# Kernel tuning notes

Measured on AMD Instinct MI355X. Metric: run time of the kernel, lower is better.

The kernel has to match this reference:

```python
import jax, jax.numpy as jnp
import numpy as np

S, B, E, H, V, L = 512, 64, 512, 768, 32000, 32
PAD_WORD, PAD_LABEL = 1, 0
PAD_BIAS = 10000.0


def _linear_init(key, fin, fout):
    # matches torch nn.Linear default U(-1/sqrt(fin), 1/sqrt(fin))
    kw, kb = jax.random.split(key)
    s = 1.0 / np.sqrt(fin)
    W = jax.random.uniform(kw, (fin, fout), minval=-s, maxval=s, dtype=jnp.float32)
    b = jax.random.uniform(kb, (fout,), minval=-s, maxval=s, dtype=jnp.float32)
    return W, b


def setup_inputs() -> dict:
    key = jax.random.key(0)
    ks = jax.random.split(key, 9)
    tokens = jax.random.randint(ks[0], (S, B), 0, V, dtype=jnp.int32)
    tags = jax.random.randint(ks[1], (S, B), 0, L, dtype=jnp.int32)
    embedding = jax.random.normal(ks[2], (V, E), dtype=jnp.float32)
    # gate order along the 4H axis: r, f, g, o (matches the 8 separate Linears, stacked)
    Wi_f, bi_f = _linear_init(ks[3], E, 4 * H)
    Wh_f, bh_f = _linear_init(ks[4], H, 4 * H)
    Wi_b, bi_b = _linear_init(ks[5], E, 4 * H)
    Wh_b, bh_b = _linear_init(ks[6], H, 4 * H)
    Wout, bout = _linear_init(ks[7], 2 * H, L)
    return {"tokens": tokens, "tags": tags, "embedding": embedding,
            "Wi_f": Wi_f, "bi_f": bi_f, "Wh_f": Wh_f, "bh_f": bh_f,
            "Wi_b": Wi_b, "bi_b": bi_b, "Wh_b": Wh_b, "bh_b": bh_b,
            "Wout": Wout, "bout": bout}


def _forward(tokens, embedding, Wi_f, bi_f, Wh_f, bh_f, Wi_b, bi_b, Wh_b, bh_b, Wout, bout):
    emb = embedding[tokens]                      # [S,B,E]
    b = tokens.shape[1]
    h = emb.shape[-1] * 0 + Wh_f.shape[0]
    # ---- forward direction: true LSTM-style recurrence ----
    xf = jnp.einsum('sbe,eg->sbg', emb, Wi_f) + bi_f   # [S,B,4H] precomputed input gates

    def step_f(carry, x):
        hid, c = carry
        g = x + hid @ Wh_f + bh_f
        r, f, gg, o = jnp.split(g, 4, axis=-1)
        c = jax.nn.sigmoid(f) * c + jax.nn.sigmoid(r) * jnp.tanh(gg)
        hid = jax.nn.sigmoid(o) * jnp.tanh(c)
        return (hid, c), hid

    z = jnp.zeros((b, h), dtype=emb.dtype)
    (hT, _), hs_f = jax.lax.scan(step_f, (z, z), xf)   # hs_f: [S,B,H]

    # ---- backward direction: source never updates `hidden`, so the hidden
    # projection uses the CONSTANT final forward hidden hT at every step.
    gb = jnp.einsum('sbe,eg->sbg', emb, Wi_b) + bi_b + hT @ Wh_b + bh_b  # [S,B,4H]
    r2, f2, g2, o2 = jnp.split(gb, 4, axis=-1)
    r2 = jax.nn.sigmoid(r2); f2 = jax.nn.sigmoid(f2)
    g2 = jnp.tanh(g2);       o2 = jax.nn.sigmoid(o2)

    def step_b(c2, gates):
        r, f, g, o = gates
        c2 = f * c2 + r * g
        return c2, o * jnp.tanh(c2)

    _, hs_b = jax.lax.scan(step_b, z, (r2, f2, g2, o2), reverse=True)  # [S,B,H], original order

    outputs = jnp.concatenate([hs_f, hs_b], axis=-1)   # [S,B,2H]
    out = outputs @ Wout + bout                        # [S,B,L]
    pad_mask = (tokens == PAD_WORD).astype(out.dtype)
    out = out.at[:, :, PAD_LABEL].add(pad_mask * PAD_BIAS)
    return out


def reference(tokens, tags, embedding, Wi_f, bi_f, Wh_f, bh_f, Wi_b, bi_b, Wh_b, bh_b, Wout, bout):
    del tags  # unused in forward, kept for signature fidelity
    return _forward(tokens, embedding, Wi_f, bi_f, Wh_f, bh_f, Wi_b, bi_b, Wh_b, bh_b, Wout, bout)
```

## Files before the change

kernel.cpp:

```cpp
#include <hip/hip_runtime.h>
#include <hip/hip_bf16.h>
#include <stdint.h>

typedef __attribute__((ext_vector_type(8))) short bf16x8;
typedef __attribute__((ext_vector_type(4))) float f32x4;
typedef __attribute__((ext_vector_type(4))) unsigned int u32x4;
typedef unsigned long long ull_t;

#define S_LEN 512
#define B_DIM 64
#define E_DIM 512
#define H_DIM 768
#define G4    3072
#define H2    1536
#define M_ROWS 32768
#define CHUNK 128
#define CM    8192
#define SLW   24
#define WPS   8
#define WPR   256
#define RWRD  4096
#define PSTR  16384
#define KRES  640
#define KREG  4
#define WROW  648
#define NTILES 1536

__device__ __forceinline__ float sigmf_(float x) { return 1.0f / (1.0f + __expf(-x)); }
__device__ __forceinline__ float tanhf2(float x) {
  x = fminf(fmaxf(x, -20.0f), 20.0f);
  float e = __expf(2.0f * x);
  return (e - 1.0f) / (e + 1.0f);
}
__device__ __forceinline__ float bfu(unsigned short u) { return __uint_as_float((unsigned)u << 16); }
__device__ __forceinline__ unsigned short packbf(float a) {
  __hip_bfloat16 t = __float2bfloat16(a);
  unsigned short b;
  __builtin_memcpy(&b, &t, 2);
  return b;
}

__global__ __launch_bounds__(256) void k_gather(const int* __restrict__ tokens,
                                                const float* __restrict__ emb,
                                                __hip_bfloat16* __restrict__ out) {
  const int t = blockIdx.x * 256 + threadIdx.x;
  const int e0 = t * 8;
  const int row = e0 >> 9;
  const int k = e0 & 511;
  const int tok = tokens[row];
  const float4* p = (const float4*)(emb + (size_t)tok * E_DIM + k);
  const float4 v0 = p[0], v1 = p[1];
  __align__(16) __hip_bfloat16 tmp[8];
  tmp[0] = __float2bfloat16(v0.x); tmp[1] = __float2bfloat16(v0.y);
  tmp[2] = __float2bfloat16(v0.z); tmp[3] = __float2bfloat16(v0.w);
  tmp[4] = __float2bfloat16(v1.x); tmp[5] = __float2bfloat16(v1.y);
  tmp[6] = __float2bfloat16(v1.z); tmp[7] = __float2bfloat16(v1.w);
  *(bf16x8*)(out + (size_t)t * 8) = *(const bf16x8*)tmp;
}

__global__ __launch_bounds__(256) void k_transpose_cast(const float* __restrict__ src,
                                                        __hip_bfloat16* __restrict__ dst,
                                                        int Rs, int Cs) {
  __shared__ float tile[32][33];
  const int tx = threadIdx.x & 31, ty = threadIdx.x >> 5;
  const int c0 = blockIdx.x * 32, r0 = blockIdx.y * 32;
  #pragma unroll
  for (int i = ty; i < 32; i += 8)
    tile[i][tx] = src[(size_t)(r0 + i) * Cs + c0 + tx];
  __syncthreads();
  #pragma unroll
  for (int i = ty; i < 32; i += 8)
    dst[(size_t)(c0 + i) * Rs + r0 + tx] = __float2bfloat16(tile[tx][i]);
}

__global__ __launch_bounds__(256) void k_bias(const float* __restrict__ bi,
                                              const float* __restrict__ bh,
                                              float* __restrict__ bias) {
  const int n = blockIdx.x * 256 + threadIdx.x;
  bias[n] = bi[n] + bh[n];
}

__device__ __forceinline__ void gemm_tile_e(char* pool, int tile,
                                            const __hip_bfloat16* __restrict__ A,
                                            const __hip_bfloat16* __restrict__ BT,
                                            const float* __restrict__ bias,
                                            __hip_bfloat16* __restrict__ C) {
  auto As = (__hip_bfloat16 (*)[40])pool;
  auto Bs = (__hip_bfloat16 (*)[40])(pool + 10240);
  const int tid = threadIdx.x;
  const int wave = tid >> 6, lane = tid & 63;
  const int q = lane >> 4, lr = lane & 15;
  const int wm = (wave >> 1) * 64, wn = (wave & 1) * 64;
  const int nb = tile % 24, mb = tile / 24;
  const int m0 = mb * 128, n0 = nb * 128;
  const int srow = tid >> 2, skseg = (tid & 3) * 8;

  f32x4 acc[4][4];
  #pragma unroll
  for (int i = 0; i < 4; ++i)
    #pragma unroll
    for (int j = 0; j < 4; ++j) { f32x4 z = {0.f, 0.f, 0.f, 0.f}; acc[i][j] = z; }

  for (int kt = 0; kt < 16; ++kt) {
    __syncthreads();
    const int kbase = kt * 32 + skseg;
    *(bf16x8*)&As[srow][skseg]      = *(const bf16x8*)(A + (size_t)(m0 + srow) * E_DIM + kbase);
    *(bf16x8*)&As[srow + 64][skseg] = *(const bf16x8*)(A + (size_t)(m0 + srow + 64) * E_DIM + kbase);
    *(bf16x8*)&Bs[srow][skseg]      = *(const bf16x8*)(BT + (size_t)(n0 + srow) * E_DIM + kbase);
    *(bf16x8*)&Bs[srow + 64][skseg] = *(const bf16x8*)(BT + (size_t)(n0 + srow + 64) * E_DIM + kbase);
    __syncthreads();
    bf16x8 af[4], bfr[4];
    #pragma unroll
    for (int mt = 0; mt < 4; ++mt) af[mt] = *(const bf16x8*)&As[wm + mt * 16 + lr][q * 8];
    #pragma unroll
    for (int nt = 0; nt < 4; ++nt) bfr[nt] = *(const bf16x8*)&Bs[wn + nt * 16 + lr][q * 8];
    #pragma unroll
    for (int mt = 0; mt < 4; ++mt)
      #pragma unroll
      for (int nt = 0; nt < 4; ++nt)
        acc[mt][nt] = __builtin_amdgcn_mfma_f32_16x16x32_bf16(af[mt], bfr[nt], acc[mt][nt], 0, 0, 0);
  }
  #pragma unroll
  for (int mt = 0; mt < 4; ++mt) {
    #pragma unroll
    for (int nt = 0; nt < 4; ++nt) {
      const int col = n0 + wn + nt * 16 + lr;
      const float bv = bias[col];
      #pragma unroll
      for (int i = 0; i < 4; ++i) {
        const int row = m0 + wm + mt * 16 + q * 4 + i;
        C[(size_t)row * G4 + col] = __float2bfloat16(acc[mt][nt][i] + bv);
      }
    }
  }
}

__device__ __forceinline__ void gemm_tile_g(char* pool, int tile,
                                            const int* __restrict__ tokens_c,
                                            const float* __restrict__ emb,
                                            const __hip_bfloat16* __restrict__ BT,
                                            const float* __restrict__ bias,
                                            __hip_bfloat16* __restrict__ C) {
  auto As = (__hip_bfloat16 (*)[40])pool;
  auto Bs = (__hip_bfloat16 (*)[40])(pool + 10240);
  const int tid = threadIdx.x;
  const int wave = tid >> 6, lane = tid & 63;
  const int q = lane >> 4, lr = lane & 15;
  const int wm = (wave >> 1) * 64, wn = (wave & 1) * 64;
  const int nb = tile % 24, mb = tile / 24;
  const int m0 = mb * 128, n0 = nb * 128;
  const int srow = tid >> 2, skseg = (tid & 3) * 8;
  const int tok0 = tokens_c[m0 + srow];
  const int tok1 = tokens_c[m0 + srow + 64];

  f32x4 acc[4][4];
  #pragma unroll
  for (int i = 0; i < 4; ++i)
    #pragma unroll
    for (int j = 0; j < 4; ++j) { f32x4 z = {0.f, 0.f, 0.f, 0.f}; acc[i][j] = z; }

  for (int kt = 0; kt < 16; ++kt) {
    __syncthreads();
    const int kbase = kt * 32 + skseg;
    {
      const float* ap = emb + (size_t)tok0 * E_DIM + kbase;
      const float4 v0 = *(const float4*)ap, v1 = *(const float4*)(ap + 4);
      __align__(16) __hip_bfloat16 t8[8];
      t8[0] = __float2bfloat16(v0.x); t8[1] = __float2bfloat16(v0.y);
      t8[2] = __float2bfloat16(v0.z); t8[3] = __float2bfloat16(v0.w);
      t8[4] = __float2bfloat16(v1.x); t8[5] = __float2bfloat16(v1.y);
      t8[6] = __float2bfloat16(v1.z); t8[7] = __float2bfloat16(v1.w);
      *(bf16x8*)&As[srow][skseg] = *(const bf16x8*)t8;
    }
    {
      const float* ap = emb + (size_t)tok1 * E_DIM + kbase;
      const float4 v0 = *(const float4*)ap, v1 = *(const float4*)(ap + 4);
      __align__(16) __hip_bfloat16 t8[8];
      t8[0] = __float2bfloat16(v0.x); t8[1] = __float2bfloat16(v0.y);
      t8[2] = __float2bfloat16(v0.z); t8[3] = __float2bfloat16(v0.w);
      t8[4] = __float2bfloat16(v1.x); t8[5] = __float2bfloat16(v1.y);
      t8[6] = __float2bfloat16(v1.z); t8[7] = __float2bfloat16(v1.w);
      *(bf16x8*)&As[srow + 64][skseg] = *(const bf16x8*)t8;
    }
    *(bf16x8*)&Bs[srow][skseg]      = *(const bf16x8*)(BT + (size_t)(n0 + srow) * E_DIM + kbase);
    *(bf16x8*)&Bs[srow + 64][skseg] = *(const bf16x8*)(BT + (size_t)(n0 + srow + 64) * E_DIM + kbase);
    __syncthreads();
    bf16x8 af[4], bfr[4];
    #pragma unroll
    for (int mt = 0; mt < 4; ++mt) af[mt] = *(const bf16x8*)&As[wm + mt * 16 + lr][q * 8];
    #pragma unroll
    for (int nt = 0; nt < 4; ++nt) bfr[nt] = *(const bf16x8*)&Bs[wn + nt * 16 + lr][q * 8];
    #pragma unroll
    for (int mt = 0; mt < 4; ++mt)
      #pragma unroll
      for (int nt = 0; nt < 4; ++nt)
        acc[mt][nt] = __builtin_amdgcn_mfma_f32_16x16x32_bf16(af[mt], bfr[nt], acc[mt][nt], 0, 0, 0);
  }
  #pragma unroll
  for (int mt = 0; mt < 4; ++mt) {
    #pragma unroll
    for (int nt = 0; nt < 4; ++nt) {
      const int col = n0 + wn + nt * 16 + lr;
      const float bv = bias[col];
      #pragma unroll
      for (int i = 0; i < 4; ++i) {
        const int row = m0 + wm + mt * 16 + q * 4 + i;
        C[(size_t)row * G4 + col] = __float2bfloat16(acc[mt][nt][i] + bv);
      }
    }
  }
}

__global__ __launch_bounds__(256) void k_gemm_e(const __hip_bfloat16* __restrict__ A,
                                                const __hip_bfloat16* __restrict__ BT,
                                                const float* __restrict__ bias,
                                                __hip_bfloat16* __restrict__ C) {
  __shared__ __align__(16) char pool[20480];
  gemm_tile_e(pool, blockIdx.x, A, BT, bias, C);
}
__global__ __launch_bounds__(256) void k_gemm_g(const int* __restrict__ tokens_c,
                                                const float* __restrict__ emb,
                                                const __hip_bfloat16* __restrict__ BT,
                                                const float* __restrict__ bias,
                                                __hip_bfloat16* __restrict__ C) {
  __shared__ __align__(16) char pool[20480];
  gemm_tile_g(pool, blockIdx.x, tokens_c, emb, BT, bias, C);
}

__device__ __forceinline__ void out_block8(char* pool, int ob,
                                           const __hip_bfloat16* __restrict__ Hs,
                                           const float* __restrict__ Wout,
                                           const float* __restrict__ bout,
                                           const int* __restrict__ tokens,
                                           float* __restrict__ out) {
  auto rowbuf = (float (*)[1536])pool;
  const int r0 = ob * 8;
  const int tid = threadIdx.x;
  for (int idx = tid; idx < 8 * 1536; idx += 256) {
    const int rr = idx / 1536, k = idx % 1536;
    rowbuf[rr][k] = __bfloat162float(Hs[(size_t)(r0 + rr) * H2 + k]);
  }
  __syncthreads();
  const int l = tid & 31, rr = tid >> 5;
  float acc = bout[l];
  #pragma unroll 8
  for (int k = 0; k < 1536; ++k) acc += rowbuf[rr][k] * Wout[k * 32 + l];
  const int row = r0 + rr;
  if (l == 0 && tokens[row] == 1) acc += 10000.0f;
  out[(size_t)row * 32 + l] = acc;
  __syncthreads();
}

__global__ __launch_bounds__(256) void k_out(const __hip_bfloat16* __restrict__ Hs,
                                             const float* __restrict__ Wout,
                                             const float* __restrict__ bout,
                                             const int* __restrict__ tokens,
                                             float* __restrict__ out) {
  __shared__ __align__(16) char pool[49152];
  out_block8(pool, blockIdx.x, Hs, Wout, bout, tokens, out);
}

__global__ __launch_bounds__(256, 1) void k_fwd_fused(const __hip_bfloat16* __restrict__ X,
                                                      const __hip_bfloat16* __restrict__ WhTf,
                                                      ull_t* __restrict__ hbuf,
                                                      __hip_bfloat16* __restrict__ Hs,
                                                      float* __restrict__ cstate,
                                                      float* __restrict__ hT,
                                                      int chunk,
                                                      const __hip_bfloat16* __restrict__ EmbA,
                                                      const int* __restrict__ tokens_nx,
                                                      const float* __restrict__ emb,
                                                      const __hip_bfloat16* __restrict__ WiT_nx,
                                                      const float* __restrict__ Bias_nx,
                                                      __hip_bfloat16* __restrict__ Xw) {
  __shared__ __align__(16) char pool[155904];
  const int bx = blockIdx.x;

  if (bx >= 128) {
    const int nw = gridDim.x - 128;
    if (EmbA) {
      for (int t = bx - 128; t < NTILES; t += nw)
        gemm_tile_e(pool, t, EmbA, WiT_nx, Bias_nx, Xw);
    } else {
      for (int t = bx - 128; t < NTILES; t += nw)
        gemm_tile_g(pool, t, tokens_nx, emb, WiT_nx, Bias_nx, Xw);
    }
    return;
  }

  unsigned short* wlds = (unsigned short*)pool;
  auto h_stage = (unsigned short (*)[776])(pool + 124416);
  auto g_lds   = (float (*)[16][26])(pool + 149248);

  const int group = bx >> 5;
  const int slice = bx & 31;
  const int r0 = group * 16;
  const int j0 = slice * SLW;
  const int tid = threadIdx.x;
  const int w = tid >> 6;
  const int lane = tid & 63;
  const int q = lane >> 4, lr = lane & 15;
  const int base = chunk * CHUNK;

  const int prow = tid >> 4;
  const int pw   = tid & 15;

  const int row  = tid >> 3;
  const int wloc = tid & 7;
  const int col0 = 3 * wloc;

  for (int c = tid; c < 96 * (KRES / 8); c += 256) {
    const int r = c / (KRES / 8), k8 = c % (KRES / 8);
    const int gate = r / SLW, n = r % SLW;
    const float4 v = *(const float4*)(WhTf + (size_t)(gate * H_DIM + j0 + n) * H_DIM + k8 * 8);
    *(float4*)(wlds + (size_t)r * WROW + k8 * 8) = v;
  }

  const int wn0 = lr;
  const int wn1 = 16 + (lr & 7);
  bf16x8 wr0[KREG], wr1[KREG];
  #pragma unroll
  for (int kk = 0; kk < KREG; ++kk) {
    const int ko = KRES + kk * 32 + q * 8;
    wr0[kk] = *(const bf16x8*)(WhTf + (size_t)(w * H_DIM + j0 + wn0) * H_DIM + ko);
    wr1[kk] = *(const bf16x8*)(WhTf + (size_t)(w * H_DIM + j0 + wn1) * H_DIM + ko);
  }

  float cr[3] = {0.f, 0.f, 0.f};
  if (tid < 128) {
    const float* cs = cstate + (size_t)(r0 + row) * H_DIM + j0 + col0;
    cr[0] = cs[0]; cr[1] = cs[1]; cr[2] = cs[2];
  }

  const unsigned skipbit = ((pw >> 2) == (slice & 3)) ? (1u << (slice >> 2)) : 0u;

  __syncthreads();

  for (int s = 0; s < CHUNK; ++s) {
    const int gs = base + s;

    unsigned short xs[4][3];
    if (tid < 128) {
      const unsigned short* xp = (const unsigned short*)(X + ((size_t)s * B_DIM + r0 + row) * G4 + j0 + col0);
      #pragma unroll
      for (int g = 0; g < 4; ++g)
        #pragma unroll
        for (int j = 0; j < 3; ++j) xs[g][j] = xp[g * H_DIM + j];
    }

    const ull_t* hc = hbuf + ((size_t)(gs & 1)) * PSTR + (size_t)group * RWRD
                    + (size_t)prow * WPR + 2 * pw;
    u32x4 d0 = {0,0,0,0}, d1 = {0,0,0,0}, d2 = {0,0,0,0}, d3 = {0,0,0,0};
    u32x4 d4 = {0,0,0,0}, d5 = {0,0,0,0}, d6 = {0,0,0,0}, d7 = {0,0,0,0};
    const unsigned pollmask = (s == 0) ? 0xFFu : (0xFFu ^ skipbit);
    {
      const unsigned e16 = (unsigned)(unsigned short)gs;
      unsigned need = pollmask;
      long guard = 0;
      for (;;) {
#define POLL_LD(i, dv) \
        if (need & (1u << (i))) \
          asm volatile("global_load_dwordx4 %0, %1, off sc0 sc1" \
                       : "=v"(dv) : "v"(hc + 32 * (i)) : "memory");
        POLL_LD(0, d0) POLL_LD(1, d1) POLL_LD(2, d2) POLL_LD(3, d3)
        POLL_LD(4, d4) POLL_LD(5, d5) POLL_LD(6, d6) POLL_LD(7, d7)
#undef POLL_LD
        asm volatile("s_waitcnt vmcnt(0)"
                     : "+v"(d0), "+v"(d1), "+v"(d2), "+v"(d3),
                       "+v"(d4), "+v"(d5), "+v"(d6), "+v"(d7)
                     :: "memory");
        unsigned nn = 0;
#define POLL_CK(i, dv) \
        if ((need & (1u << (i))) && \
            ((((dv).x & 0xFFFFu) != e16) || (((dv).z & 0xFFFFu) != e16))) nn |= 1u << (i);
        POLL_CK(0, d0) POLL_CK(1, d1) POLL_CK(2, d2) POLL_CK(3, d3)
        POLL_CK(4, d4) POLL_CK(5, d5) POLL_CK(6, d6) POLL_CK(7, d7)
#undef POLL_CK
        need = nn;
        if (!need) break;
        if (++guard > (1L << 20)) break;
        __builtin_amdgcn_s_sleep(1);
      }
    }
    {
#define STAGE_PAIR(i, dv) \
      if (pollmask & (1u << (i))) { \
        unsigned* hp = (unsigned*)&h_stage[prow][6 * pw + 96 * (i)]; \
        hp[0] = ((dv).x >> 16) | ((dv).y << 16); \
        hp[1] = ((dv).y >> 16) | ((dv).z & 0xFFFF0000u); \
        hp[2] = (dv).w; \
      }
      STAGE_PAIR(0, d0) STAGE_PAIR(1, d1) STAGE_PAIR(2, d2) STAGE_PAIR(3, d3)
      STAGE_PAIR(4, d4) STAGE_PAIR(5, d5) STAGE_PAIR(6, d6) STAGE_PAIR(7, d7)
#undef STAGE_PAIR
    }
    __syncthreads();

    f32x4 acc0 = {0.f, 0.f, 0.f, 0.f};
    f32x4 acc1 = {0.f, 0.f, 0.f, 0.f};
    {
      const unsigned short* wb = wlds + (size_t)w * SLW * WROW;
      #pragma unroll
      for (int kt = 0; kt < KRES / 32; ++kt) {
        const int ko = kt * 32 + q * 8;
        const bf16x8 a  = *(const bf16x8*)&h_stage[lr][ko];
        const bf16x8 b0 = *(const bf16x8*)(wb + (size_t)wn0 * WROW + ko);
        const bf16x8 b1 = *(const bf16x8*)(wb + (size_t)wn1 * WROW + ko);
        acc0 = __builtin_amdgcn_mfma_f32_16x16x32_bf16(a, b0, acc0, 0, 0, 0);
        acc1 = __builtin_amdgcn_mfma_f32_16x16x32_bf16(a, b1, acc1, 0, 0, 0);
      }
      #pragma unroll
      for (int kk = 0; kk < KREG; ++kk) {
        const bf16x8 a = *(const bf16x8*)&h_stage[lr][KRES + kk * 32 + q * 8];
        acc0 = __builtin_amdgcn_mfma_f32_16x16x32_bf16(a, wr0[kk], acc0, 0, 0, 0);
        acc1 = __builtin_amdgcn_mfma_f32_16x16x32_bf16(a, wr1[kk], acc1, 0, 0, 0);
      }
    }
    #pragma unroll
    for (int i = 0; i < 4; ++i) g_lds[w][q * 4 + i][lr] = acc0[i];
    if (lr < 8) {
      #pragma unroll
      for (int i = 0; i < 4; ++i) g_lds[w][q * 4 + i][16 + lr] = acc1[i];
    }
    __syncthreads();

    if (tid < 128) {
      float h[3];
      #pragma unroll
      for (int j = 0; j < 3; ++j) {
        const float rv = g_lds[0][row][col0 + j] + bfu(xs[0][j]);
        const float fv = g_lds[1][row][col0 + j] + bfu(xs[1][j]);
        const float gv = g_lds[2][row][col0 + j] + bfu(xs[2][j]);
        const float ov = g_lds[3][row][col0 + j] + bfu(xs[3][j]);
        const float c = sigmf_(fv) * cr[j] + sigmf_(rv) * tanhf2(gv);
        cr[j] = c;
        h[j] = sigmf_(ov) * tanhf2(c);
      }
      const unsigned short b0 = packbf(h[0]), b1 = packbf(h[1]), b2 = packbf(h[2]);
      const ull_t wv = (ull_t)(unsigned short)(gs + 1)
                     | ((ull_t)b0 << 16) | ((ull_t)b1 << 32) | ((ull_t)b2 << 48);
      __hip_atomic_store(hbuf + ((size_t)((gs + 1) & 1)) * PSTR + (size_t)group * RWRD
                         + (size_t)row * WPR + slice * WPS + wloc,
                         wv, __ATOMIC_RELAXED, __HIP_MEMORY_SCOPE_AGENT);
      h_stage[row][j0 + col0]     = b0;
      h_stage[row][j0 + col0 + 1] = b1;
      h_stage[row][j0 + col0 + 2] = b2;
      unsigned short* hsp = (unsigned short*)(Hs + ((size_t)gs * B_DIM + r0 + row) * H2 + j0 + col0);
      hsp[0] = b0; hsp[1] = b1; hsp[2] = b2;
      if (chunk == 3 && s == CHUNK - 1) {
        float* hp = hT + (size_t)(r0 + row) * H_DIM + j0 + col0;
        hp[0] = h[0]; hp[1] = h[1]; hp[2] = h[2];
      }
    }
  }

  if (tid < 128) {
    float* cs = cstate + (size_t)(r0 + row) * H_DIM + j0 + col0;
    cs[0] = cr[0]; cs[1] = cr[1]; cs[2] = cr[2];
  }
}

__global__ __launch_bounds__(256) void k_hTW(const float* __restrict__ hT,
                                             const float* __restrict__ Whb,
                                             float* __restrict__ hTW) {
  const int b = blockIdx.y;
  const int n = blockIdx.x * 256 + threadIdx.x;
  __shared__ float hs[768];
  for (int i = threadIdx.x; i < 768; i += 256) hs[i] = hT[b * 768 + i];
  __syncthreads();
  float acc = 0.f;
  #pragma unroll 4
  for (int k = 0; k < 768; ++k) acc += hs[k] * Whb[(size_t)k * G4 + n];
  hTW[(size_t)b * G4 + n] = acc;
}

__global__ __launch_bounds__(256) void k_bwd_fused(const __hip_bfloat16* __restrict__ X,
                                                   const float* __restrict__ hTW,
                                                   __hip_bfloat16* __restrict__ Hs,
                                                   float* __restrict__ c2state,
                                                   int chunk,
                                                   const __hip_bfloat16* __restrict__ EmbB,
                                                   const int* __restrict__ tokens_nx,
                                                   const float* __restrict__ emb,
                                                   const __hip_bfloat16* __restrict__ WiTb,
                                                   const float* __restrict__ BiasB,
                                                   __hip_bfloat16* __restrict__ Xw,
                                                   int do_gemm, int out_chunk,
                                                   const float* __restrict__ Wout,
                                                   const float* __restrict__ bout,
                                                   const int* __restrict__ tokens_all,
                                                   float* __restrict__ out) {
  __shared__ __align__(16) char pool[49152];
  const int bx = blockIdx.x;

  if (bx >= 640) {
    if (out_chunk >= 0)
      for (int ob = bx - 640; ob < 1024; ob += 128)
        out_block8(pool, out_chunk * 1024 + ob, Hs, Wout, bout, tokens_all, out);
    return;
  }
  if (bx >= 192) {
    if (do_gemm) {
      if (EmbB) {
        for (int t = bx - 192; t < NTILES; t += 448)
          gemm_tile_e(pool, t, EmbB, WiTb, BiasB, Xw);
      } else {
        for (int t = bx - 192; t < NTILES; t += 448)
          gemm_tile_g(pool, t, tokens_nx, emb, WiTb, BiasB, Xw);
      }
    }
    return;
  }

  const int t = bx * 256 + threadIdx.x;
  const int b = t / H_DIM;
  const int j = t % H_DIM;
  const int base = chunk * CHUNK;
  const float hw0 = hTW[(size_t)b * G4 + j];
  const float hw1 = hTW[(size_t)b * G4 + 768 + j];
  const float hw2 = hTW[(size_t)b * G4 + 1536 + j];
  const float hw3 = hTW[(size_t)b * G4 + 2304 + j];
  float c2 = c2state[t];
  for (int s = CHUNK - 1; s >= 0; --s) {
    const size_t xb = ((size_t)s * B_DIM + b) * G4 + j;
    const float r = sigmf_(__bfloat162float(X[xb]) + hw0);
    const float f = sigmf_(__bfloat162float(X[xb + 768]) + hw1);
    const float g = tanhf2(__bfloat162float(X[xb + 1536]) + hw2);
    const float o = sigmf_(__bfloat162float(X[xb + 2304]) + hw3);
    c2 = f * c2 + r * g;
    Hs[((size_t)(base + s) * B_DIM + b) * H2 + H_DIM + j] = __float2bfloat16(o * tanhf2(c2));
  }
  c2state[t] = c2;
}

extern "C" void kernel_launch(void* const* d_in, const int* in_sizes, int n_in,
                              void* d_out, int out_size, void* d_ws, size_t ws_size,
                              hipStream_t stream) {
  const int*   tokens = (const int*)d_in[0];
  const float* emb    = (const float*)d_in[2];
  const float* Wi_f   = (const float*)d_in[3];
  const float* bi_f   = (const float*)d_in[4];
  const float* Wh_f   = (const float*)d_in[5];
  const float* bh_f   = (const float*)d_in[6];
  const float* Wi_b   = (const float*)d_in[7];
  const float* bi_b   = (const float*)d_in[8];
  const float* Wh_b   = (const float*)d_in[9];
  const float* bh_b   = (const float*)d_in[10];
  const float* Wout   = (const float*)d_in[11];
  const float* bout   = (const float*)d_in[12];
  float* out = (float*)d_out;
  char* ws = (char*)d_ws;

  size_t off = 0;
  auto alloc = [&](size_t bytes) { size_t o = off; off += (bytes + 255) & ~(size_t)255; return o; };
  const size_t oHs    = alloc((size_t)M_ROWS * H2 * 2);
  const size_t oX0    = alloc((size_t)CM * G4 * 2);
  const size_t oWhTf  = alloc((size_t)G4 * H_DIM * 2);
  const size_t oWiTf  = alloc((size_t)G4 * E_DIM * 2);
  const size_t oWiTb  = alloc((size_t)G4 * E_DIM * 2);
  const size_t oBiasF = alloc((size_t)G4 * 4);
  const size_t oBiasB = alloc((size_t)G4 * 4);
  const size_t oHbuf  = alloc((size_t)2 * PSTR * 8);
  const size_t oCst   = alloc((size_t)B_DIM * H_DIM * 4);
  const size_t oHT    = alloc((size_t)B_DIM * H_DIM * 4);
  const size_t oHTW   = alloc((size_t)B_DIM * G4 * 4);
  const size_t oC2    = alloc((size_t)B_DIM * H_DIM * 4);
  const size_t oX1    = alloc((size_t)CM * G4 * 2);
  const bool overlap = (off <= ws_size);
  const size_t oEmb   = alloc((size_t)M_ROWS * E_DIM * 2);
  const bool tierA = (off <= ws_size);
  (void)in_sizes; (void)n_in; (void)out_size;

  __hip_bfloat16* Hs   = (__hip_bfloat16*)(ws + oHs);
  __hip_bfloat16* X0   = (__hip_bfloat16*)(ws + oX0);
  __hip_bfloat16* X1   = overlap ? (__hip_bfloat16*)(ws + oX1) : X0;
  __hip_bfloat16* Emb  = tierA ? (__hip_bfloat16*)(ws + oEmb) : (__hip_bfloat16*)nullptr;
  __hip_bfloat16* WhTf = (__hip_bfloat16*)(ws + oWhTf);
  __hip_bfloat16* WiTf = (__hip_bfloat16*)(ws + oWiTf);
  __hip_bfloat16* WiTb = (__hip_bfloat16*)(ws + oWiTb);
  float*          BiasF= (float*)(ws + oBiasF);
  float*          BiasB= (float*)(ws + oBiasB);
  ull_t*          Hbuf = (ull_t*)(ws + oHbuf);
  float*          Cst  = (float*)(ws + oCst);
  float*          HT   = (float*)(ws + oHT);
  float*          HTW  = (float*)(ws + oHTW);
  float*          C2   = (float*)(ws + oC2);

  hipMemsetAsync(ws + oHbuf, 0, (size_t)2 * PSTR * 8, stream);
  hipMemsetAsync(ws + oCst, 0, (size_t)B_DIM * H_DIM * 4, stream);
  hipMemsetAsync(ws + oC2, 0, (size_t)B_DIM * H_DIM * 4, stream);

  if (tierA)
    k_gather<<<8192, 256, 0, stream>>>(tokens, emb, Emb);
  k_transpose_cast<<<dim3(96, 24), 256, 0, stream>>>(Wh_f, WhTf, 768, 3072);
  k_transpose_cast<<<dim3(96, 16), 256, 0, stream>>>(Wi_f, WiTf, 512, 3072);
  k_transpose_cast<<<dim3(96, 16), 256, 0, stream>>>(Wi_b, WiTb, 512, 3072);
  k_bias<<<12, 256, 0, stream>>>(bi_f, bh_f, BiasF);
  k_bias<<<12, 256, 0, stream>>>(bi_b, bh_b, BiasB);

  if (overlap) {
    if (tierA) k_gemm_e<<<NTILES, 256, 0, stream>>>(Emb, WiTf, BiasF, X0);
    else       k_gemm_g<<<NTILES, 256, 0, stream>>>(tokens, emb, WiTf, BiasF, X0);
    auto EA = [&](int c) { return tierA ? Emb + (size_t)c * CM * E_DIM : (__hip_bfloat16*)nullptr; };
    k_fwd_fused<<<240, 256, 0, stream>>>(X0, WhTf, Hbuf, Hs, Cst, HT, 0,
                                         EA(1), tokens + 1 * CM, emb, WiTf, BiasF, X1);
    k_fwd_fused<<<240, 256, 0, stream>>>(X1, WhTf, Hbuf, Hs, Cst, HT, 1,
                                         EA(2), tokens + 2 * CM, emb, WiTf, BiasF, X0);
    k_fwd_fused<<<240, 256, 0, stream>>>(X0, WhTf, Hbuf, Hs, Cst, HT, 2,
                                         EA(3), tokens + 3 * CM, emb, WiTf, BiasF, X1);
    k_fwd_fused<<<240, 256, 0, stream>>>(X1, WhTf, Hbuf, Hs, Cst, HT, 3,
                                         EA(3), tokens + 3 * CM, emb, WiTb, BiasB, X0);
    k_hTW<<<dim3(12, 64), 256, 0, stream>>>(HT, Wh_b, HTW);
    k_bwd_fused<<<768, 256, 0, stream>>>(X0, HTW, Hs, C2, 3,
                                         EA(2), tokens + 2 * CM, emb, WiTb, BiasB, X1, 1, -1,
                                         Wout, bout, tokens, out);
    k_bwd_fused<<<768, 256, 0, stream>>>(X1, HTW, Hs, C2, 2,
                                         EA(1), tokens + 1 * CM, emb, WiTb, BiasB, X0, 1, 3,
                                         Wout, bout, tokens, out);
    k_bwd_fused<<<768, 256, 0, stream>>>(X0, HTW, Hs, C2, 1,
                                         EA(0), tokens + 0 * CM, emb, WiTb, BiasB, X1, 1, 2,
                                         Wout, bout, tokens, out);
    k_bwd_fused<<<768, 256, 0, stream>>>(X1, HTW, Hs, C2, 0,
                                         EA(0), tokens, emb, WiTb, BiasB, X0, 0, 1,
                                         Wout, bout, tokens, out);
    k_out<<<1024, 256, 0, stream>>>(Hs, Wout, bout, tokens, out);
  } else {
    for (int c = 0; c < 4; ++c) {
      k_gemm_g<<<NTILES, 256, 0, stream>>>(tokens + (size_t)c * CM, emb, WiTf, BiasF, X0);
      k_fwd_fused<<<128, 256, 0, stream>>>(X0, WhTf, Hbuf, Hs, Cst, HT, c,
                                           nullptr, tokens, emb, WiTf, BiasF, X0);
    }
    k_hTW<<<dim3(12, 64), 256, 0, stream>>>(HT, Wh_b, HTW);
    for (int c = 3; c >= 0; --c) {
      k_gemm_g<<<NTILES, 256, 0, stream>>>(tokens + (size_t)c * CM, emb, WiTb, BiasB, X0);
      k_bwd_fused<<<192, 256, 0, stream>>>(X0, HTW, Hs, C2, c,
                                           nullptr, tokens, emb, WiTb, BiasB, X0, 0, -1,
                                           Wout, bout, tokens, out);
    }
    k_out<<<4096, 256, 0, stream>>>(Hs, Wout, bout, tokens, out);
  }
}
```

Baseline: 3.292 ms.

## Fuse backward input-gate GEMM into backward scan, dropping X gate buffer

Replaces the backward pass, which first materialised the input-gate projection X and then scanned it, with a kernel that keeps a 96x512 slice of Wi_b resident in LDS. At each step pair it loads embeddings and computes the gate pre-activations with MFMA before applying the cell update in place. This removes the global write and reread of the large bf16 gate tensor and the separate GEMM tiles in the backward pass. In exchange it uses about 143 KB of LDS per block, runs one block per CU, and serialises each step on block-wide barriers. The separate backward GEMM is also no longer prefetched by the last forward launch.

```diff
diff --git a/kernel.cpp b/kernel.cpp
--- a/kernel.cpp
+++ b/kernel.cpp
@@ -25,6 +25,7 @@
 #define KREG  4
 #define WROW  648
 #define NTILES 1536
+#define EROW  520
 
 __device__ __forceinline__ float sigmf_(float x) { return 1.0f / (1.0f + __expf(-x)); }
 __device__ __forceinline__ float tanhf2(float x) {
@@ -474,45 +475,139 @@
   hTW[(size_t)b * G4 + n] = acc;
 }
 
-__global__ __launch_bounds__(256) void k_bwd_fused(const __hip_bfloat16* __restrict__ X,
-                                                   const float* __restrict__ hTW,
-                                                   __hip_bfloat16* __restrict__ Hs,
-                                                   float* __restrict__ c2state,
-                                                   int chunk,
-                                                   const __hip_bfloat16* __restrict__ EmbB,
-                                                   const int* __restrict__ tokens_nx,
-                                                   const float* __restrict__ emb,
-                                                   const __hip_bfloat16* __restrict__ WiTb,
-                                                   const float* __restrict__ BiasB,
-                                                   __hip_bfloat16* __restrict__ Xw,
-                                                   int do_gemm, int out_chunk,
-                                                   const float* __restrict__ Wout,
-                                                   const float* __restrict__ bout,
-                                                   const int* __restrict__ tokens_all,
-                                                   float* __restrict__ out) {
-  __shared__ __align__(16) char pool[49152];
+__global__ __launch_bounds__(256, 1) void k_bwd_fused2(const __hip_bfloat16* __restrict__ Emb,
+                                                       const __hip_bfloat16* __restrict__ WiTb,
+                                                       const float* __restrict__ BiasB,
+                                                       const float* __restrict__ hTW,
+                                                       __hip_bfloat16* __restrict__ Hs,
+                                                       float* __restrict__ c2state,
+                                                       int chunk, int out_chunk,
+                                                       const float* __restrict__ Wout,
+                                                       const float* __restrict__ bout,
+                                                       const int* __restrict__ tokens,
+                                                       float* __restrict__ out) {
+  __shared__ __align__(16) char pool[146432];
   const int bx = blockIdx.x;
 
-  if (bx >= 640) {
+  if (bx >= 128) {
     if (out_chunk >= 0)
-      for (int ob = bx - 640; ob < 1024; ob += 128)
-        out_block8(pool, out_chunk * 1024 + ob, Hs, Wout, bout, tokens_all, out);
+      for (int ob = bx - 128; ob < 1024; ob += 128)
+        out_block8(pool, out_chunk * 1024 + ob, Hs, Wout, bout, tokens, out);
     return;
   }
-  if (bx >= 192) {
-    if (do_gemm) {
-      if (EmbB) {
-        for (int t = bx - 192; t < NTILES; t += 448)
-          gemm_tile_e(pool, t, EmbB, WiTb, BiasB, Xw);
-      } else {
-        for (int t = bx - 192; t < NTILES; t += 448)
-          gemm_tile_g(pool, t, tokens_nx, emb, WiTb, BiasB, Xw);
-      }
-    }
-    return;
-  }
-
-  const int t = bx * 256 + threadIdx.x;
+
+  unsigned short* wlds = (unsigned short*)pool;
+  auto emb_s = (unsigned short (*)[EROW])(pool + 99840);
+  auto g_lds = (float (*)[2][16][26])(pool + 133120);
+
+  const int group = bx >> 5;
+  const int slice = bx & 31;
+  const int r0 = group * 16;
+  const int j0 = slice * SLW;
+  const int tid = threadIdx.x;
+  const int w = tid >> 6;
+  const int lane = tid & 63;
+  const int q = lane >> 4, lr = lane & 15;
+  const int base = chunk * CHUNK;
+
+  for (int c = tid; c < 96 * 64; c += 256) {
+    const int r = c >> 6, k8 = c & 63;
+    const int gate = r / SLW, n = r % SLW;
+    *(float4*)(wlds + (size_t)r * EROW + k8 * 8) =
+        *(const float4*)(WiTb + (size_t)(gate * H_DIM + j0 + n) * E_DIM + k8 * 8);
+  }
+
+  const int row = tid >> 3, wloc = tid & 7, col0 = 3 * wloc;
+  float hw0[3], hw1[3], hw2[3], hw3[3], c2r[3] = {0.f, 0.f, 0.f};
+  if (tid < 128) {
+    const int b = r0 + row;
+    #pragma unroll
+    for (int j = 0; j < 3; ++j) {
+      const int n = j0 + col0 + j;
+      hw0[j] = BiasB[n]        + hTW[(size_t)b * G4 + n];
+      hw1[j] = BiasB[768 + n]  + hTW[(size_t)b * G4 + 768 + n];
+      hw2[j] = BiasB[1536 + n] + hTW[(size_t)b * G4 + 1536 + n];
+      hw3[j] = BiasB[2304 + n] + hTW[(size_t)b * G4 + 2304 + n];
+      c2r[j] = c2state[(size_t)b * H_DIM + n];
+    }
+  }
+  const int wn0 = lr;
+  const int wn1 = 16 + (lr & 7);
+  const unsigned short* wb0 = wlds + (size_t)(w * SLW + wn0) * EROW;
+  const unsigned short* wb1 = wlds + (size_t)(w * SLW + wn1) * EROW;
+  __syncthreads();
+
+  for (int t = CHUNK / 2 - 1; t >= 0; --t) {
+    for (int c = tid; c < 32 * 64; c += 256) {
+      const int a = c >> 6, k8 = c & 63;
+      const int ss = 2 * t + 1 - (a >> 4);
+      *(float4*)(&emb_s[a][k8 * 8]) =
+          *(const float4*)(Emb + ((size_t)(base + ss) * B_DIM + r0 + (a & 15)) * E_DIM + k8 * 8);
+    }
+    __syncthreads();
+
+    f32x4 a00 = {0.f,0.f,0.f,0.f}, a01 = {0.f,0.f,0.f,0.f};
+    f32x4 a10 = {0.f,0.f,0.f,0.f}, a11 = {0.f,0.f,0.f,0.f};
+    #pragma unroll
+    for (int kt = 0; kt < 16; ++kt) {
+      const int ko = kt * 32 + q * 8;
+      const bf16x8 b0 = *(const bf16x8*)(wb0 + ko);
+      const bf16x8 b1 = *(const bf16x8*)(wb1 + ko);
+      const bf16x8 aA = *(const bf16x8*)(&emb_s[lr][ko]);
+      const bf16x8 aB = *(const bf16x8*)(&emb_s[16 + lr][ko]);
+      a00 = __builtin_amdgcn_mfma_f32_16x16x32_bf16(aA, b0, a00, 0, 0, 0);
+      a01 = __builtin_amdgcn_mfma_f32_16x16x32_bf16(aA, b1, a01, 0, 0, 0);
+      a10 = __builtin_amdgcn_mfma_f32_16x16x32_bf16(aB, b0, a10, 0, 0, 0);
+      a11 = __builtin_amdgcn_mfma_f32_16x16x32_bf16(aB, b1, a11, 0, 0, 0);
+    }
+    #pragma unroll
+    for (int i = 0; i < 4; ++i) {
+      g_lds[w][0][q * 4 + i][lr] = a00[i];
+      g_lds[w][1][q * 4 + i][lr] = a10[i];
+    }
+    if (lr < 8) {
+      #pragma unroll
+      for (int i = 0; i < 4; ++i) {
+        g_lds[w][0][q * 4 + i][16 + lr] = a01[i];
+        g_lds[w][1][q * 4 + i][16 + lr] = a11[i];
+      }
+    }
+    __syncthreads();
+
+    if (tid < 128) {
+      #pragma unroll
+      for (int st = 0; st < 2; ++st) {
+        const int gs = base + 2 * t + 1 - st;
+        unsigned short hb[3];
+        #pragma unroll
+        for (int j = 0; j < 3; ++j) {
+          const float rv = sigmf_(g_lds[0][st][row][col0 + j] + hw0[j]);
+          const float fv = sigmf_(g_lds[1][st][row][col0 + j] + hw1[j]);
+          const float gv = tanhf2(g_lds[2][st][row][col0 + j] + hw2[j]);
+          const float ov = sigmf_(g_lds[3][st][row][col0 + j] + hw3[j]);
+          c2r[j] = fv * c2r[j] + rv * gv;
+          hb[j] = packbf(ov * tanhf2(c2r[j]));
+        }
+        unsigned short* hsp = (unsigned short*)(Hs + ((size_t)gs * B_DIM + r0 + row) * H2
+                                                + H_DIM + j0 + col0);
+        hsp[0] = hb[0]; hsp[1] = hb[1]; hsp[2] = hb[2];
+      }
+    }
+  }
+
+  if (tid < 128) {
+    #pragma unroll
+    for (int j = 0; j < 3; ++j)
+      c2state[(size_t)(r0 + row) * H_DIM + j0 + col0 + j] = c2r[j];
+  }
+}
+
+__global__ __launch_bounds__(256) void k_bwd_scan(const __hip_bfloat16* __restrict__ X,
+                                                  const float* __restrict__ hTW,
+                                                  __hip_bfloat16* __restrict__ Hs,
+                                                  float* __restrict__ c2state,
+                                                  int chunk) {
+  const int t = blockIdx.x * 256 + threadIdx.x;
   const int b = t / H_DIM;
   const int j = t % H_DIM;
   const int base = chunk * CHUNK;
@@ -598,32 +693,44 @@
   k_bias<<<12, 256, 0, stream>>>(bi_f, bh_f, BiasF);
   k_bias<<<12, 256, 0, stream>>>(bi_b, bh_b, BiasB);
 
-  if (overlap) {
-    if (tierA) k_gemm_e<<<NTILES, 256, 0, stream>>>(Emb, WiTf, BiasF, X0);
-    else       k_gemm_g<<<NTILES, 256, 0, stream>>>(tokens, emb, WiTf, BiasF, X0);
-    auto EA = [&](int c) { return tierA ? Emb + (size_t)c * CM * E_DIM : (__hip_bfloat16*)nullptr; };
+  if (overlap && tierA) {
+    k_gemm_e<<<NTILES, 256, 0, stream>>>(Emb, WiTf, BiasF, X0);
+    auto EA = [&](int c) { return Emb + (size_t)c * CM * E_DIM; };
     k_fwd_fused<<<240, 256, 0, stream>>>(X0, WhTf, Hbuf, Hs, Cst, HT, 0,
-                                         EA(1), tokens + 1 * CM, emb, WiTf, BiasF, X1);
+                                         EA(1), tokens, emb, WiTf, BiasF, X1);
     k_fwd_fused<<<240, 256, 0, stream>>>(X1, WhTf, Hbuf, Hs, Cst, HT, 1,
-                                         EA(2), tokens + 2 * CM, emb, WiTf, BiasF, X0);
+                                         EA(2), tokens, emb, WiTf, BiasF, X0);
     k_fwd_fused<<<240, 256, 0, stream>>>(X0, WhTf, Hbuf, Hs, Cst, HT, 2,
-                                         EA(3), tokens + 3 * CM, emb, WiTf, BiasF, X1);
+                                         EA(3), tokens, emb, WiTf, BiasF, X1);
+    k_fwd_fused<<<128, 256, 0, stream>>>(X1, WhTf, Hbuf, Hs, Cst, HT, 3,
+                                         EA(0), tokens, emb, WiTf, BiasF, X0);
+    k_hTW<<<dim3(12, 64), 256, 0, stream>>>(HT, Wh_b, HTW);
+    k_bwd_fused2<<<256, 256, 0, stream>>>(Emb, WiTb, BiasB, HTW, Hs, C2, 3, -1,
+                                          Wout, bout, tokens, out);
+    k_bwd_fused2<<<256, 256, 0, stream>>>(Emb, WiTb, BiasB, HTW, Hs, C2, 2, 3,
+                                          Wout, bout, tokens, out);
+    k_bwd_fused2<<<256, 256, 0, stream>>>(Emb, WiTb, BiasB, HTW, Hs, C2, 1, 2,
+                                          Wout, bout, tokens, out);
+    k_bwd_fused2<<<256, 256, 0, stream>>>(Emb, WiTb, BiasB, HTW, Hs, C2, 0, 1,
+                                          Wout, bout, tokens, out);
+    k_out<<<1024, 256, 0, stream>>>(Hs, Wout, bout, tokens, out);
+  } else if (overlap) {
+    k_gemm_g<<<NTILES, 256, 0, stream>>>(tokens, emb, WiTf, BiasF, X0);
+    k_fwd_fused<<<240, 256, 0, stream>>>(X0, WhTf, Hbuf, Hs, Cst, HT, 0,
+                                         nullptr, tokens + 1 * CM, emb, WiTf, BiasF, X1);
+    k_fwd_fused<<<240, 256, 0, stream>>>(X1, WhTf, Hbuf, Hs, Cst, HT, 1,
+                                         nullptr, tokens + 2 * CM, emb, WiTf, BiasF, X0);
+    k_fwd_fused<<<240, 256, 0, stream>>>(X0, WhTf, Hbuf, Hs, Cst, HT, 2,
+                                         nullptr, tokens + 3 * CM, emb, WiTf, BiasF, X1);
     k_fwd_fused<<<240, 256, 0, stream>>>(X1, WhTf, Hbuf, Hs, Cst, HT, 3,
-                                         EA(3), tokens + 3 * CM, emb, WiTb, BiasB, X0);
+                                         nullptr, tokens + 3 * CM, emb, WiTb, BiasB, X0);
     k_hTW<<<dim3(12, 64), 256, 0, stream>>>(HT, Wh_b, HTW);
-    k_bwd_fused<<<768, 256, 0, stream>>>(X0, HTW, Hs, C2, 3,
-                                         EA(2), tokens + 2 * CM, emb, WiTb, BiasB, X1, 1, -1,
-                                         Wout, bout, tokens, out);
-    k_bwd_fused<<<768, 256, 0, stream>>>(X1, HTW, Hs, C2, 2,
-                                         EA(1), tokens + 1 * CM, emb, WiTb, BiasB, X0, 1, 3,
-                                         Wout, bout, tokens, out);
-    k_bwd_fused<<<768, 256, 0, stream>>>(X0, HTW, Hs, C2, 1,
-                                         EA(0), tokens + 0 * CM, emb, WiTb, BiasB, X1, 1, 2,
-                                         Wout, bout, tokens, out);
-    k_bwd_fused<<<768, 256, 0, stream>>>(X1, HTW, Hs, C2, 0,
-                                         EA(0), tokens, emb, WiTb, BiasB, X0, 0, 1,
-                                         Wout, bout, tokens, out);
-    k_out<<<1024, 256, 0, stream>>>(Hs, Wout, bout, tokens, out);
+    k_bwd_scan<<<192, 256, 0, stream>>>(X0, HTW, Hs, C2, 3);
+    for (int c = 2; c >= 0; --c) {
+      k_gemm_g<<<NTILES, 256, 0, stream>>>(tokens + (size_t)c * CM, emb, WiTb, BiasB, X1);
+      k_bwd_scan<<<192, 256, 0, stream>>>(X1, HTW, Hs, C2, c);
+    }
+    k_out<<<4096, 256, 0, stream>>>(Hs, Wout, bout, tokens, out);
   } else {
     for (int c = 0; c < 4; ++c) {
       k_gemm_g<<<NTILES, 256, 0, stream>>>(tokens + (size_t)c * CM, emb, WiTf, BiasF, X0);
@@ -633,9 +740,7 @@
     k_hTW<<<dim3(12, 64), 256, 0, stream>>>(HT, Wh_b, HTW);
     for (int c = 3; c >= 0; --c) {
       k_gemm_g<<<NTILES, 256, 0, stream>>>(tokens + (size_t)c * CM, emb, WiTb, BiasB, X0);
-      k_bwd_fused<<<192, 256, 0, stream>>>(X0, HTW, Hs, C2, c,
-                                           nullptr, tokens, emb, WiTb, BiasB, X0, 0, -1,
-                                           Wout, bout, tokens, out);
+      k_bwd_scan<<<192, 256, 0, stream>>>(X0, HTW, Hs, C2, c);
     }
     k_out<<<4096, 256, 0, stream>>>(Hs, Wout, bout, tokens, out);
   }
```

Measured after the change: 3.594 ms. 9.2% more time.
